# Kernel optimization log

Measured on AMD Instinct MI355X. Metric: run time of the kernel, lower is better.

Reference implementation:

```python
import jax, jax.numpy as jnp
import numpy as np


def setup_inputs() -> dict:
    key = jax.random.key(0)
    k1, k2, k3, k4 = jax.random.split(key, 4)
    B, E, V, K = 2048, 1024, 100000, 128
    receiver_output = jax.random.normal(k1, (B, E), dtype=jnp.float32)
    emb = jax.random.normal(k2, (V, E), dtype=jnp.float32)
    nns = jax.random.randint(k3, (V, K), 0, V, dtype=jnp.int64)
    labels = jax.random.randint(k4, (B,), 0, V, dtype=jnp.int64)
    return {
        "receiver_output": receiver_output,
        "emb": emb,
        "nns": nns,
        "labels": labels,
        "num_hard_negatives": 127,
    }


def reference(receiver_output, emb, nns, labels, num_hard_negatives):
    # Gather hard-negative neighbor ids: (B, K) with K = num_hard_negatives + 1.
    batch_nns = nns[labels][:, : num_hard_negatives + 1]
    # Gather neighbor embeddings: (B, K, E).
    batch_emb = emb[batch_nns]
    # L2-normalize receiver output.
    ro = receiver_output / jnp.linalg.norm(receiver_output, axis=-1, keepdims=True)
    # Batched cosine logits: (B, K). Target class is always index 0.
    receiver_cosine = jnp.einsum("bne,be->bn", batch_emb, ro)
    # Cross entropy with label 0, reduction='none' -> (B,).
    loss = -jax.nn.log_softmax(receiver_cosine, axis=-1)[:, 0]
    # acc as in original: argmax of normalized receiver_output over dim 1 vs zero labels.
    acc = (jnp.argmax(ro, axis=1) == 0).astype(jnp.float32)
    return loss, acc
```

## Files before the change

kernel.cpp:

```cpp
#include <hip/hip_runtime.h>
#include <math.h>

#define THREADS 256
#define NWAVES (THREADS / 64)

__global__ __launch_bounds__(THREADS) void disc_loss_kernel(
    const float* __restrict__ ro_g,
    const float* __restrict__ emb,
    const int* __restrict__ nns,
    const int* __restrict__ labels,
    const int* __restrict__ nhn_ptr,
    float* __restrict__ loss_out,
    float* __restrict__ acc_out,
    int E, int Knns)
{
    const int b    = blockIdx.x;
    const int tid  = threadIdx.x;
    const int lane = tid & 63;
    const int wave = tid >> 6;
    const int K    = nhn_ptr[0] + 1;
    const int E4   = E >> 2;

    extern __shared__ char smem_raw[];
    float* s_ro     = (float*)smem_raw;
    float* s_scores = s_ro + E;
    int*   s_nns    = (int*)(s_scores + Knns);
    __shared__ float s_sum[NWAVES], s_max[NWAVES];
    __shared__ float s_invnorm;

    const float4* ro4   = (const float4*)(ro_g + (size_t)b * E);
    float4*       s_ro4 = (float4*)s_ro;
    float lsum = 0.f, lmax = -INFINITY;
    for (int i = tid; i < E4; i += THREADS) {
        float4 v = ro4[i];
        s_ro4[i] = v;
        lsum += v.x * v.x + v.y * v.y + v.z * v.z + v.w * v.w;
        lmax = fmaxf(lmax, fmaxf(fmaxf(v.x, v.y), fmaxf(v.z, v.w)));
    }

    const int label = labels[b];
    const int* nrow = nns + (size_t)label * Knns;
    for (int i = tid; i < K; i += THREADS) s_nns[i] = nrow[i];

    for (int m = 32; m; m >>= 1) {
        lsum += __shfl_xor(lsum, m, 64);
        lmax = fmaxf(lmax, __shfl_xor(lmax, m, 64));
    }
    if (lane == 0) { s_sum[wave] = lsum; s_max[wave] = lmax; }
    __syncthreads();
    if (tid == 0) {
        float t = 0.f, mx = -INFINITY;
        for (int w = 0; w < NWAVES; ++w) { t += s_sum[w]; mx = fmaxf(mx, s_max[w]); }
        s_invnorm = 1.0f / sqrtf(t);
        acc_out[b] = (s_ro[0] >= mx) ? 1.0f : 0.0f;
    }
    __syncthreads();
    const float invn = s_invnorm;

    for (int n = wave; n < K; n += 2 * NWAVES) {
        const int n1   = n + NWAVES;
        const int idx0 = s_nns[n];
        const int idx1 = (n1 < K) ? s_nns[n1] : idx0;
        const float4* e0 = (const float4*)(emb + (size_t)idx0 * E);
        const float4* e1 = (const float4*)(emb + (size_t)idx1 * E);

        float acc0 = 0.f, acc1 = 0.f;
        int j = lane;
        for (; j + 192 < E4; j += 256) {
            float4 a0 = e0[j], a1 = e0[j + 64], a2 = e0[j + 128], a3 = e0[j + 192];
            float4 b0 = e1[j], b1 = e1[j + 64], b2 = e1[j + 128], b3 = e1[j + 192];
            float4 r0 = s_ro4[j], r1 = s_ro4[j + 64], r2 = s_ro4[j + 128], r3 = s_ro4[j + 192];
            acc0 += a0.x * r0.x + a0.y * r0.y + a0.z * r0.z + a0.w * r0.w;
            acc0 += a1.x * r1.x + a1.y * r1.y + a1.z * r1.z + a1.w * r1.w;
            acc0 += a2.x * r2.x + a2.y * r2.y + a2.z * r2.z + a2.w * r2.w;
            acc0 += a3.x * r3.x + a3.y * r3.y + a3.z * r3.z + a3.w * r3.w;
            acc1 += b0.x * r0.x + b0.y * r0.y + b0.z * r0.z + b0.w * r0.w;
            acc1 += b1.x * r1.x + b1.y * r1.y + b1.z * r1.z + b1.w * r1.w;
            acc1 += b2.x * r2.x + b2.y * r2.y + b2.z * r2.z + b2.w * r2.w;
            acc1 += b3.x * r3.x + b3.y * r3.y + b3.z * r3.z + b3.w * r3.w;
        }
        for (; j < E4; j += 64) {
            float4 a = e0[j], c = e1[j], r = s_ro4[j];
            acc0 += a.x * r.x + a.y * r.y + a.z * r.z + a.w * r.w;
            acc1 += c.x * r.x + c.y * r.y + c.z * r.z + c.w * r.w;
        }
        for (int m = 32; m; m >>= 1) {
            acc0 += __shfl_xor(acc0, m, 64);
            acc1 += __shfl_xor(acc1, m, 64);
        }
        if (lane == 0) {
            s_scores[n] = acc0 * invn;
            if (n1 < K) s_scores[n1] = acc1 * invn;
        }
    }
    __syncthreads();

    if (wave == 0) {
        float v0 = (lane < K) ? s_scores[lane] : -INFINITY;
        float v1 = (lane + 64 < K) ? s_scores[lane + 64] : -INFINITY;
        float m = fmaxf(v0, v1);
        for (int mm = 32; mm; mm >>= 1) m = fmaxf(m, __shfl_xor(m, mm, 64));
        float e = ((lane < K) ? expf(v0 - m) : 0.f) +
                  ((lane + 64 < K) ? expf(v1 - m) : 0.f);
        for (int mm = 32; mm; mm >>= 1) e += __shfl_xor(e, mm, 64);
        if (lane == 0) loss_out[b] = logf(e) + m - s_scores[0];
    }
}

extern "C" void kernel_launch(void* const* d_in, const int* in_sizes, int n_in,
                              void* d_out, int out_size, void* d_ws, size_t ws_size,
                              hipStream_t stream) {
    const float* ro     = (const float*)d_in[0];
    const float* emb    = (const float*)d_in[1];
    const int*   nns    = (const int*)d_in[2];
    const int*   labels = (const int*)d_in[3];
    const int*   nhn    = (const int*)d_in[4];

    const int B    = in_sizes[3];
    const int E    = in_sizes[0] / B;
    const int V    = in_sizes[1] / E;
    const int Knns = in_sizes[2] / V;

    float* loss_out = (float*)d_out;
    float* acc_out  = loss_out + B;

    size_t smem = (size_t)(E + Knns) * sizeof(float) + (size_t)Knns * sizeof(int);
    disc_loss_kernel<<<dim3(B), dim3(THREADS), smem, stream>>>(
        ro, emb, nns, labels, nhn, loss_out, acc_out, E, Knns);
}
```

Baseline: 624.5 us.

## Keep receiver row in registers and process four neighbors per wave

```diff
diff --git a/kernel.cpp b/kernel.cpp
--- a/kernel.cpp
+++ b/kernel.cpp
@@ -2,8 +2,9 @@
 #include <math.h>
 
 #define THREADS 256
-#define NWAVES (THREADS / 64)
-
+#define NWAVES 4
+
+template <int NCHUNK>
 __global__ __launch_bounds__(THREADS) void disc_loss_kernel(
     const float* __restrict__ ro_g,
     const float* __restrict__ emb,
@@ -19,78 +20,66 @@
     const int lane = tid & 63;
     const int wave = tid >> 6;
     const int K    = nhn_ptr[0] + 1;
-    const int E4   = E >> 2;
-
-    extern __shared__ char smem_raw[];
-    float* s_ro     = (float*)smem_raw;
-    float* s_scores = s_ro + E;
-    int*   s_nns    = (int*)(s_scores + Knns);
-    __shared__ float s_sum[NWAVES], s_max[NWAVES];
-    __shared__ float s_invnorm;
-
-    const float4* ro4   = (const float4*)(ro_g + (size_t)b * E);
-    float4*       s_ro4 = (float4*)s_ro;
+
+    __shared__ float s_scores[256];
+    __shared__ int   s_nns[256];
+
+    const int  label = labels[b];
+    const int* nrow  = nns + (size_t)label * Knns;
+    for (int i = tid; i < K; i += THREADS) s_nns[i] = nrow[i];
+
+    const float4* ro4 = (const float4*)(ro_g + (size_t)b * E);
+    float4 r[NCHUNK];
     float lsum = 0.f, lmax = -INFINITY;
-    for (int i = tid; i < E4; i += THREADS) {
-        float4 v = ro4[i];
-        s_ro4[i] = v;
+#pragma unroll
+    for (int c = 0; c < NCHUNK; ++c) {
+        float4 v = ro4[lane + 64 * c];
+        r[c] = v;
         lsum += v.x * v.x + v.y * v.y + v.z * v.z + v.w * v.w;
         lmax = fmaxf(lmax, fmaxf(fmaxf(v.x, v.y), fmaxf(v.z, v.w)));
     }
-
-    const int label = labels[b];
-    const int* nrow = nns + (size_t)label * Knns;
-    for (int i = tid; i < K; i += THREADS) s_nns[i] = nrow[i];
-
     for (int m = 32; m; m >>= 1) {
         lsum += __shfl_xor(lsum, m, 64);
         lmax = fmaxf(lmax, __shfl_xor(lmax, m, 64));
     }
-    if (lane == 0) { s_sum[wave] = lsum; s_max[wave] = lmax; }
-    __syncthreads();
-    if (tid == 0) {
-        float t = 0.f, mx = -INFINITY;
-        for (int w = 0; w < NWAVES; ++w) { t += s_sum[w]; mx = fmaxf(mx, s_max[w]); }
-        s_invnorm = 1.0f / sqrtf(t);
-        acc_out[b] = (s_ro[0] >= mx) ? 1.0f : 0.0f;
-    }
-    __syncthreads();
-    const float invn = s_invnorm;
-
-    for (int n = wave; n < K; n += 2 * NWAVES) {
-        const int n1   = n + NWAVES;
-        const int idx0 = s_nns[n];
-        const int idx1 = (n1 < K) ? s_nns[n1] : idx0;
-        const float4* e0 = (const float4*)(emb + (size_t)idx0 * E);
-        const float4* e1 = (const float4*)(emb + (size_t)idx1 * E);
-
-        float acc0 = 0.f, acc1 = 0.f;
-        int j = lane;
-        for (; j + 192 < E4; j += 256) {
-            float4 a0 = e0[j], a1 = e0[j + 64], a2 = e0[j + 128], a3 = e0[j + 192];
-            float4 b0 = e1[j], b1 = e1[j + 64], b2 = e1[j + 128], b3 = e1[j + 192];
-            float4 r0 = s_ro4[j], r1 = s_ro4[j + 64], r2 = s_ro4[j + 128], r3 = s_ro4[j + 192];
-            acc0 += a0.x * r0.x + a0.y * r0.y + a0.z * r0.z + a0.w * r0.w;
-            acc0 += a1.x * r1.x + a1.y * r1.y + a1.z * r1.z + a1.w * r1.w;
-            acc0 += a2.x * r2.x + a2.y * r2.y + a2.z * r2.z + a2.w * r2.w;
-            acc0 += a3.x * r3.x + a3.y * r3.y + a3.z * r3.z + a3.w * r3.w;
-            acc1 += b0.x * r0.x + b0.y * r0.y + b0.z * r0.z + b0.w * r0.w;
-            acc1 += b1.x * r1.x + b1.y * r1.y + b1.z * r1.z + b1.w * r1.w;
-            acc1 += b2.x * r2.x + b2.y * r2.y + b2.z * r2.z + b2.w * r2.w;
-            acc1 += b3.x * r3.x + b3.y * r3.y + b3.z * r3.z + b3.w * r3.w;
-        }
-        for (; j < E4; j += 64) {
-            float4 a = e0[j], c = e1[j], r = s_ro4[j];
-            acc0 += a.x * r.x + a.y * r.y + a.z * r.z + a.w * r.w;
-            acc1 += c.x * r.x + c.y * r.y + c.z * r.z + c.w * r.w;
+    const float invn = 1.0f / sqrtf(lsum);
+    if (tid == 0)
+        acc_out[b] = (ro_g[(size_t)b * E] >= lmax) ? 1.0f : 0.0f;
+
+    __syncthreads();
+
+    for (int n0 = wave * 4; n0 < K; n0 += NWAVES * 4) {
+        const int i0 = s_nns[n0];
+        const int i1 = s_nns[(n0 + 1 < K) ? n0 + 1 : n0];
+        const int i2 = s_nns[(n0 + 2 < K) ? n0 + 2 : n0];
+        const int i3 = s_nns[(n0 + 3 < K) ? n0 + 3 : n0];
+        const float4* e0 = (const float4*)(emb + (size_t)i0 * E);
+        const float4* e1 = (const float4*)(emb + (size_t)i1 * E);
+        const float4* e2 = (const float4*)(emb + (size_t)i2 * E);
+        const float4* e3 = (const float4*)(emb + (size_t)i3 * E);
+
+        float a0 = 0.f, a1 = 0.f, a2 = 0.f, a3 = 0.f;
+#pragma unroll
+        for (int c = 0; c < NCHUNK; ++c) {
+            const int j = lane + 64 * c;
+            float4 v0 = e0[j], v1 = e1[j], v2 = e2[j], v3 = e3[j];
+            float4 rc = r[c];
+            a0 += v0.x * rc.x + v0.y * rc.y + v0.z * rc.z + v0.w * rc.w;
+            a1 += v1.x * rc.x + v1.y * rc.y + v1.z * rc.z + v1.w * rc.w;
+            a2 += v2.x * rc.x + v2.y * rc.y + v2.z * rc.z + v2.w * rc.w;
+            a3 += v3.x * rc.x + v3.y * rc.y + v3.z * rc.z + v3.w * rc.w;
         }
         for (int m = 32; m; m >>= 1) {
-            acc0 += __shfl_xor(acc0, m, 64);
-            acc1 += __shfl_xor(acc1, m, 64);
+            a0 += __shfl_xor(a0, m, 64);
+            a1 += __shfl_xor(a1, m, 64);
+            a2 += __shfl_xor(a2, m, 64);
+            a3 += __shfl_xor(a3, m, 64);
         }
         if (lane == 0) {
-            s_scores[n] = acc0 * invn;
-            if (n1 < K) s_scores[n1] = acc1 * invn;
+            s_scores[n0] = a0 * invn;
+            if (n0 + 1 < K) s_scores[n0 + 1] = a1 * invn;
+            if (n0 + 2 < K) s_scores[n0 + 2] = a2 * invn;
+            if (n0 + 3 < K) s_scores[n0 + 3] = a3 * invn;
         }
     }
     __syncthreads();
@@ -107,6 +96,82 @@
     }
 }
 
+__global__ __launch_bounds__(THREADS) void disc_loss_kernel_generic(
+    const float* __restrict__ ro_g,
+    const float* __restrict__ emb,
+    const int* __restrict__ nns,
+    const int* __restrict__ labels,
+    const int* __restrict__ nhn_ptr,
+    float* __restrict__ loss_out,
+    float* __restrict__ acc_out,
+    int E, int Knns)
+{
+    const int b    = blockIdx.x;
+    const int tid  = threadIdx.x;
+    const int lane = tid & 63;
+    const int wave = tid >> 6;
+    const int K    = nhn_ptr[0] + 1;
+    const int E4   = E >> 2;
+
+    extern __shared__ char smem_raw[];
+    float* s_ro     = (float*)smem_raw;
+    float* s_scores = s_ro + E;
+    int*   s_nns    = (int*)(s_scores + Knns);
+    __shared__ float s_sum[NWAVES], s_max[NWAVES];
+    __shared__ float s_invnorm;
+
+    const float4* ro4   = (const float4*)(ro_g + (size_t)b * E);
+    float4*       s_ro4 = (float4*)s_ro;
+    float lsum = 0.f, lmax = -INFINITY;
+    for (int i = tid; i < E4; i += THREADS) {
+        float4 v = ro4[i];
+        s_ro4[i] = v;
+        lsum += v.x * v.x + v.y * v.y + v.z * v.z + v.w * v.w;
+        lmax = fmaxf(lmax, fmaxf(fmaxf(v.x, v.y), fmaxf(v.z, v.w)));
+    }
+    const int label = labels[b];
+    const int* nrow = nns + (size_t)label * Knns;
+    for (int i = tid; i < K; i += THREADS) s_nns[i] = nrow[i];
+    for (int m = 32; m; m >>= 1) {
+        lsum += __shfl_xor(lsum, m, 64);
+        lmax = fmaxf(lmax, __shfl_xor(lmax, m, 64));
+    }
+    if (lane == 0) { s_sum[wave] = lsum; s_max[wave] = lmax; }
+    __syncthreads();
+    if (tid == 0) {
+        float t = 0.f, mx = -INFINITY;
+        for (int w = 0; w < NWAVES; ++w) { t += s_sum[w]; mx = fmaxf(mx, s_max[w]); }
+        s_invnorm = 1.0f / sqrtf(t);
+        acc_out[b] = (s_ro[0] >= mx) ? 1.0f : 0.0f;
+    }
+    __syncthreads();
+    const float invn = s_invnorm;
+
+    for (int n = wave; n < K; n += NWAVES) {
+        const int idx = s_nns[n];
+        const float4* e = (const float4*)(emb + (size_t)idx * E);
+        float acc = 0.f;
+        for (int j = lane; j < E4; j += 64) {
+            float4 a = e[j], rr = s_ro4[j];
+            acc += a.x * rr.x + a.y * rr.y + a.z * rr.z + a.w * rr.w;
+        }
+        for (int m = 32; m; m >>= 1) acc += __shfl_xor(acc, m, 64);
+        if (lane == 0) s_scores[n] = acc * invn;
+    }
+    __syncthreads();
+
+    if (wave == 0) {
+        float v0 = (lane < K) ? s_scores[lane] : -INFINITY;
+        float v1 = (lane + 64 < K) ? s_scores[lane + 64] : -INFINITY;
+        float m = fmaxf(v0, v1);
+        for (int mm = 32; mm; mm >>= 1) m = fmaxf(m, __shfl_xor(m, mm, 64));
+        float e = ((lane < K) ? expf(v0 - m) : 0.f) +
+                  ((lane + 64 < K) ? expf(v1 - m) : 0.f);
+        for (int mm = 32; mm; mm >>= 1) e += __shfl_xor(e, mm, 64);
+        if (lane == 0) loss_out[b] = logf(e) + m - s_scores[0];
+    }
+}
+
 extern "C" void kernel_launch(void* const* d_in, const int* in_sizes, int n_in,
                               void* d_out, int out_size, void* d_ws, size_t ws_size,
                               hipStream_t stream) {
@@ -124,7 +189,20 @@
     float* loss_out = (float*)d_out;
     float* acc_out  = loss_out + B;
 
-    size_t smem = (size_t)(E + Knns) * sizeof(float) + (size_t)Knns * sizeof(int);
-    disc_loss_kernel<<<dim3(B), dim3(THREADS), smem, stream>>>(
-        ro, emb, nns, labels, nhn, loss_out, acc_out, E, Knns);
+    const int nchunk = (E % 256 == 0) ? (E / 256) : 0;
+    switch (nchunk) {
+        case 1: disc_loss_kernel<1><<<dim3(B), dim3(THREADS), 0, stream>>>(
+                    ro, emb, nns, labels, nhn, loss_out, acc_out, E, Knns); break;
+        case 2: disc_loss_kernel<2><<<dim3(B), dim3(THREADS), 0, stream>>>(
+                    ro, emb, nns, labels, nhn, loss_out, acc_out, E, Knns); break;
+        case 4: disc_loss_kernel<4><<<dim3(B), dim3(THREADS), 0, stream>>>(
+                    ro, emb, nns, labels, nhn, loss_out, acc_out, E, Knns); break;
+        case 8: disc_loss_kernel<8><<<dim3(B), dim3(THREADS), 0, stream>>>(
+                    ro, emb, nns, labels, nhn, loss_out, acc_out, E, Knns); break;
+        default: {
+            size_t smem = (size_t)(E + Knns) * sizeof(float) + (size_t)Knns * sizeof(int);
+            disc_loss_kernel_generic<<<dim3(B), dim3(THREADS), smem, stream>>>(
+                ro, emb, nns, labels, nhn, loss_out, acc_out, E, Knns);
+        }
+    }
 }
```

Result: no change. 622.3 us (-0.4%).

## Invert gather: iterate embedding rows via linked lists of referencing samples

Applied to the files above, without the earlier changes.

```diff
diff --git a/kernel.cpp b/kernel.cpp
--- a/kernel.cpp
+++ b/kernel.cpp
@@ -2,46 +2,42 @@
 #include <math.h>
 
 #define THREADS 256
-#define NWAVES (THREADS / 64)
 
-__global__ __launch_bounds__(THREADS) void disc_loss_kernel(
-    const float* __restrict__ ro_g,
-    const float* __restrict__ emb,
+__global__ __launch_bounds__(THREADS) void build_lists_kernel(
     const int* __restrict__ nns,
     const int* __restrict__ labels,
     const int* __restrict__ nhn_ptr,
-    float* __restrict__ loss_out,
+    int* __restrict__ head,
+    int* __restrict__ next,
+    int B, int Knns)
+{
+    const int rid = blockIdx.x * THREADS + threadIdx.x;
+    if (rid >= B * Knns) return;
+    const int b = (unsigned)rid / (unsigned)Knns;
+    const int k = rid - b * Knns;
+    const int K = nhn_ptr[0] + 1;
+    if (k >= K) return;
+    const int v = nns[(size_t)labels[b] * Knns + k];
+    const int old = atomicExch(&head[v], rid);
+    next[rid] = old;
+}
+
+__global__ __launch_bounds__(THREADS) void row_norm_kernel(
+    const float* __restrict__ ro_g,
+    float* __restrict__ invn,
     float* __restrict__ acc_out,
-    int E, int Knns)
+    int E)
 {
-    const int b    = blockIdx.x;
-    const int tid  = threadIdx.x;
-    const int lane = tid & 63;
-    const int wave = tid >> 6;
-    const int K    = nhn_ptr[0] + 1;
-    const int E4   = E >> 2;
-
-    extern __shared__ char smem_raw[];
-    float* s_ro     = (float*)smem_raw;
-    float* s_scores = s_ro + E;
-    int*   s_nns    = (int*)(s_scores + Knns);
-    __shared__ float s_sum[NWAVES], s_max[NWAVES];
-    __shared__ float s_invnorm;
-
-    const float4* ro4   = (const float4*)(ro_g + (size_t)b * E);
-    float4*       s_ro4 = (float4*)s_ro;
+    const int b = blockIdx.x, tid = threadIdx.x, lane = tid & 63, wave = tid >> 6;
+    const int E4 = E >> 2;
+    __shared__ float s_sum[4], s_max[4];
+    const float4* ro4 = (const float4*)(ro_g + (size_t)b * E);
     float lsum = 0.f, lmax = -INFINITY;
     for (int i = tid; i < E4; i += THREADS) {
         float4 v = ro4[i];
-        s_ro4[i] = v;
         lsum += v.x * v.x + v.y * v.y + v.z * v.z + v.w * v.w;
         lmax = fmaxf(lmax, fmaxf(fmaxf(v.x, v.y), fmaxf(v.z, v.w)));
     }
-
-    const int label = labels[b];
-    const int* nrow = nns + (size_t)label * Knns;
-    for (int i = tid; i < K; i += THREADS) s_nns[i] = nrow[i];
-
     for (int m = 32; m; m >>= 1) {
         lsum += __shfl_xor(lsum, m, 64);
         lmax = fmaxf(lmax, __shfl_xor(lmax, m, 64));
@@ -50,61 +46,102 @@
     __syncthreads();
     if (tid == 0) {
         float t = 0.f, mx = -INFINITY;
-        for (int w = 0; w < NWAVES; ++w) { t += s_sum[w]; mx = fmaxf(mx, s_max[w]); }
-        s_invnorm = 1.0f / sqrtf(t);
-        acc_out[b] = (s_ro[0] >= mx) ? 1.0f : 0.0f;
+        for (int w = 0; w < 4; ++w) { t += s_sum[w]; mx = fmaxf(mx, s_max[w]); }
+        invn[b] = 1.0f / sqrtf(t);
+        acc_out[b] = (ro_g[(size_t)b * E] >= mx) ? 1.0f : 0.0f;
     }
-    __syncthreads();
-    const float invn = s_invnorm;
+}
 
-    for (int n = wave; n < K; n += 2 * NWAVES) {
-        const int n1   = n + NWAVES;
-        const int idx0 = s_nns[n];
-        const int idx1 = (n1 < K) ? s_nns[n1] : idx0;
-        const float4* e0 = (const float4*)(emb + (size_t)idx0 * E);
-        const float4* e1 = (const float4*)(emb + (size_t)idx1 * E);
+template <int NCHUNK>
+__global__ __launch_bounds__(THREADS) void gather_dot_kernel(
+    const float* __restrict__ emb,
+    const float* __restrict__ ro_g,
+    const float* __restrict__ invn,
+    const int* __restrict__ head,
+    const int* __restrict__ next,
+    float* __restrict__ scores,
+    int V, int E, int Knns)
+{
+    const int lane = threadIdx.x & 63;
+    const int wave = threadIdx.x >> 6;
+    const int v = blockIdx.x * 4 + wave;
+    if (v >= V) return;
+    int i = head[v];
+    if (i < 0) return;
 
-        float acc0 = 0.f, acc1 = 0.f;
-        int j = lane;
-        for (; j + 192 < E4; j += 256) {
-            float4 a0 = e0[j], a1 = e0[j + 64], a2 = e0[j + 128], a3 = e0[j + 192];
-            float4 b0 = e1[j], b1 = e1[j + 64], b2 = e1[j + 128], b3 = e1[j + 192];
-            float4 r0 = s_ro4[j], r1 = s_ro4[j + 64], r2 = s_ro4[j + 128], r3 = s_ro4[j + 192];
-            acc0 += a0.x * r0.x + a0.y * r0.y + a0.z * r0.z + a0.w * r0.w;
-            acc0 += a1.x * r1.x + a1.y * r1.y + a1.z * r1.z + a1.w * r1.w;
-            acc0 += a2.x * r2.x + a2.y * r2.y + a2.z * r2.z + a2.w * r2.w;
-            acc0 += a3.x * r3.x + a3.y * r3.y + a3.z * r3.z + a3.w * r3.w;
-            acc1 += b0.x * r0.x + b0.y * r0.y + b0.z * r0.z + b0.w * r0.w;
-            acc1 += b1.x * r1.x + b1.y * r1.y + b1.z * r1.z + b1.w * r1.w;
-            acc1 += b2.x * r2.x + b2.y * r2.y + b2.z * r2.z + b2.w * r2.w;
-            acc1 += b3.x * r3.x + b3.y * r3.y + b3.z * r3.z + b3.w * r3.w;
+    const float4* e4 = (const float4*)(emb + (size_t)v * E);
+    float4 r[NCHUNK];
+#pragma unroll
+    for (int c = 0; c < NCHUNK; ++c) r[c] = e4[lane + 64 * c];
+
+    while (i >= 0) {
+        const int inext = next[i];
+        const int b = (unsigned)i / (unsigned)Knns;
+        const float4* ro4 = (const float4*)(ro_g + (size_t)b * E);
+        float acc = 0.f;
+#pragma unroll
+        for (int c = 0; c < NCHUNK; ++c) {
+            float4 x = ro4[lane + 64 * c];
+            float4 rc = r[c];
+            acc += x.x * rc.x + x.y * rc.y + x.z * rc.z + x.w * rc.w;
         }
-        for (; j < E4; j += 64) {
-            float4 a = e0[j], c = e1[j], r = s_ro4[j];
-            acc0 += a.x * r.x + a.y * r.y + a.z * r.z + a.w * r.w;
-            acc1 += c.x * r.x + c.y * r.y + c.z * r.z + c.w * r.w;
+        for (int m = 32; m; m >>= 1) acc += __shfl_xor(acc, m, 64);
+        if (lane == 0) scores[i] = acc * invn[b];
+        i = inext;
+    }
+}
+
+__global__ __launch_bounds__(THREADS) void gather_dot_generic(
+    const float* __restrict__ emb,
+    const float* __restrict__ ro_g,
+    const float* __restrict__ invn,
+    const int* __restrict__ head,
+    const int* __restrict__ next,
+    float* __restrict__ scores,
+    int V, int E, int Knns)
+{
+    const int lane = threadIdx.x & 63;
+    const int wave = threadIdx.x >> 6;
+    const int v = blockIdx.x * 4 + wave;
+    if (v >= V) return;
+    int i = head[v];
+    if (i < 0) return;
+    const int E4 = E >> 2;
+    const float4* e4 = (const float4*)(emb + (size_t)v * E);
+    while (i >= 0) {
+        const int inext = next[i];
+        const int b = (unsigned)i / (unsigned)Knns;
+        const float4* ro4 = (const float4*)(ro_g + (size_t)b * E);
+        float acc = 0.f;
+        for (int j = lane; j < E4; j += 64) {
+            float4 x = ro4[j], e = e4[j];
+            acc += x.x * e.x + x.y * e.y + x.z * e.z + x.w * e.w;
         }
-        for (int m = 32; m; m >>= 1) {
-            acc0 += __shfl_xor(acc0, m, 64);
-            acc1 += __shfl_xor(acc1, m, 64);
-        }
-        if (lane == 0) {
-            s_scores[n] = acc0 * invn;
-            if (n1 < K) s_scores[n1] = acc1 * invn;
-        }
+        for (int m = 32; m; m >>= 1) acc += __shfl_xor(acc, m, 64);
+        if (lane == 0) scores[i] = acc * invn[b];
+        i = inext;
     }
-    __syncthreads();
+}
 
-    if (wave == 0) {
-        float v0 = (lane < K) ? s_scores[lane] : -INFINITY;
-        float v1 = (lane + 64 < K) ? s_scores[lane + 64] : -INFINITY;
-        float m = fmaxf(v0, v1);
-        for (int mm = 32; mm; mm >>= 1) m = fmaxf(m, __shfl_xor(m, mm, 64));
-        float e = ((lane < K) ? expf(v0 - m) : 0.f) +
-                  ((lane + 64 < K) ? expf(v1 - m) : 0.f);
-        for (int mm = 32; mm; mm >>= 1) e += __shfl_xor(e, mm, 64);
-        if (lane == 0) loss_out[b] = logf(e) + m - s_scores[0];
-    }
+__global__ __launch_bounds__(THREADS) void loss_kernel(
+    const float* __restrict__ scores,
+    const int* __restrict__ nhn_ptr,
+    float* __restrict__ loss_out,
+    int B, int Knns)
+{
+    const int lane = threadIdx.x & 63;
+    const int wave = threadIdx.x >> 6;
+    const int b = blockIdx.x * 4 + wave;
+    if (b >= B) return;
+    const int K = nhn_ptr[0] + 1;
+    const float* s = scores + (size_t)b * Knns;
+    float m = -INFINITY;
+    for (int k = lane; k < K; k += 64) m = fmaxf(m, s[k]);
+    for (int mm = 32; mm; mm >>= 1) m = fmaxf(m, __shfl_xor(m, mm, 64));
+    float e = 0.f;
+    for (int k = lane; k < K; k += 64) e += expf(s[k] - m);
+    for (int mm = 32; mm; mm >>= 1) e += __shfl_xor(e, mm, 64);
+    if (lane == 0) loss_out[b] = logf(e) + m - s[0];
 }
 
 extern "C" void kernel_launch(void* const* d_in, const int* in_sizes, int n_in,
@@ -124,7 +161,36 @@
     float* loss_out = (float*)d_out;
     float* acc_out  = loss_out + B;
 
-    size_t smem = (size_t)(E + Knns) * sizeof(float) + (size_t)Knns * sizeof(int);
-    disc_loss_kernel<<<dim3(B), dim3(THREADS), smem, stream>>>(
-        ro, emb, nns, labels, nhn, loss_out, acc_out, E, Knns);
+    char* ws = (char*)d_ws;
+    auto align = [](size_t x) { return (x + 255) & ~(size_t)255; };
+    int*   head   = (int*)ws;                         ws += align((size_t)V * 4);
+    int*   next   = (int*)ws;                         ws += align((size_t)B * Knns * 4);
+    float* invn   = (float*)ws;                       ws += align((size_t)B * 4);
+    float* scores = (float*)ws;
+
+    hipMemsetAsync(head, 0xFF, (size_t)V * sizeof(int), stream);
+
+    const int nrefs = B * Knns;
+    build_lists_kernel<<<dim3((nrefs + THREADS - 1) / THREADS), dim3(THREADS), 0, stream>>>(
+        nns, labels, nhn, head, next, B, Knns);
+
+    row_norm_kernel<<<dim3(B), dim3(THREADS), 0, stream>>>(ro, invn, acc_out, E);
+
+    const int vblocks = (V + 3) / 4;
+    const int nchunk = (E % 256 == 0) ? (E / 256) : 0;
+    switch (nchunk) {
+        case 1: gather_dot_kernel<1><<<dim3(vblocks), dim3(THREADS), 0, stream>>>(
+                    emb, ro, invn, head, next, scores, V, E, Knns); break;
+        case 2: gather_dot_kernel<2><<<dim3(vblocks), dim3(THREADS), 0, stream>>>(
+                    emb, ro, invn, head, next, scores, V, E, Knns); break;
+        case 4: gather_dot_kernel<4><<<dim3(vblocks), dim3(THREADS), 0, stream>>>(
+                    emb, ro, invn, head, next, scores, V, E, Knns); break;
+        case 8: gather_dot_kernel<8><<<dim3(vblocks), dim3(THREADS), 0, stream>>>(
+                    emb, ro, invn, head, next, scores, V, E, Knns); break;
+        default: gather_dot_generic<<<dim3(vblocks), dim3(THREADS), 0, stream>>>(
+                    emb, ro, invn, head, next, scores, V, E, Knns);
+    }
+
+    loss_kernel<<<dim3((B + 3) / 4), dim3(THREADS), 0, stream>>>(
+        scores, nhn, loss_out, B, Knns);
 }
```

Result: faster. 609.6 us (-2.4%).
